# Optimization experiments

Measured on AMD Instinct MI355X. Metric: run time of the kernel, lower is better.

The kernel has to match this reference:

```python
import jax, jax.numpy as jnp
import numpy as np

D_MODEL = 768
D_INNER = 1536   # expand=2
D_STATE = 16
D_CONV = 4
DT_RANK = 48     # ceil(768/16)
B, T, N = 2, 4, 196


def _rmsnorm(x, w, eps=1e-5):
    var = jnp.mean(x * x, axis=-1, keepdims=True)
    return x * jax.lax.rsqrt(var + eps) * w


def _causal_dwconv(x, w, b):
    # x: (b, l, di), w: (di, k) depthwise, causal left-pad k-1
    xc = jnp.swapaxes(x, 1, 2)  # (b, di, l)
    out = jax.lax.conv_general_dilated(
        xc, w[:, None, :], window_strides=(1,), padding=[(D_CONV - 1, 0)],
        feature_group_count=D_INNER, dimension_numbers=('NCH', 'OIH', 'NCH'))
    return jnp.swapaxes(out + b[None, :, None], 1, 2)


def _selective_scan(u, dt, A, Bm, Cm, Dp):
    # u, dt: (b,l,di); Bm, Cm: (b,l,n); A: (di,n); Dp: (di,)
    dA = jnp.exp(dt[..., None] * A)                    # (b,l,di,n)
    dBu = (dt * u)[..., None] * Bm[:, :, None, :]      # (b,l,di,n)

    def step(h, inp):
        dA_t, dBu_t, C_t = inp
        h = dA_t * h + dBu_t                           # (b,di,n)
        return h, jnp.einsum('bdn,bn->bd', h, C_t)

    h0 = jnp.zeros((u.shape[0], D_INNER, D_STATE), u.dtype)
    _, ys = jax.lax.scan(step, h0, (jnp.swapaxes(dA, 0, 1),
                                    jnp.swapaxes(dBu, 0, 1),
                                    jnp.swapaxes(Cm, 0, 1)))
    return jnp.swapaxes(ys, 0, 1) + u * Dp


def _mamba(x, in_w, cw, cb, xp_w, dt_w, dt_b, A_log, Dp, out_w):
    xz = jnp.einsum('blc,ec->ble', x, in_w)            # (b,l,2*di)
    xb, z = jnp.split(xz, 2, axis=-1)
    xb = jax.nn.silu(_causal_dwconv(xb, cw, cb))
    x_dbl = jnp.einsum('bld,ed->ble', xb, xp_w)        # (b,l,dt_rank+2n)
    dt, Bm, Cm = jnp.split(x_dbl, [DT_RANK, DT_RANK + D_STATE], axis=-1)
    dt = jax.nn.softplus(jnp.einsum('blr,dr->bld', dt, dt_w) + dt_b)
    y = _selective_scan(xb, dt, -jnp.exp(A_log), Bm, Cm, Dp)
    y = y * jax.nn.silu(z)
    return jnp.einsum('bld,cd->blc', y, out_w)


def _block(x, i, norm_w, in_proj_w, conv_w, conv_b, x_proj_w, dt_proj_w,
           dt_proj_b, A_log, D, mix_out_w):
    # residual Mamba block: x + mixer(norm(x)); zero-initialized ssm/conv state
    return x + _mamba(_rmsnorm(x, norm_w[i]), in_proj_w[i], conv_w[i], conv_b[i],
                      x_proj_w[i], dt_proj_w[i], dt_proj_b[i], A_log[i], D[i],
                      mix_out_w[i])


def _bimamba(x, norm_w, in_proj_w, conv_w, conv_b, x_proj_w, dt_proj_w,
             dt_proj_b, A_log, D, mix_out_w, gate_w, gate_b, proj_w, proj_b):
    b, t, n, c = x.shape
    xs = x.reshape(b, t * n, c)
    params = (norm_w, in_proj_w, conv_w, conv_b, x_proj_w, dt_proj_w,
              dt_proj_b, A_log, D, mix_out_w)
    out_f = _block(xs, 0, *params)
    flip_t = lambda y: y.reshape(b, t, n, c)[:, ::-1].reshape(b, t * n, c)
    out_b = flip_t(_block(flip_t(xs), 1, *params))
    gate = jax.nn.sigmoid(
        jnp.einsum('blc,dc->bld', jnp.concatenate([out_f, out_b], -1), gate_w)
        + gate_b)
    out = gate * out_f + (1.0 - gate) * out_b
    out = jnp.einsum('bld,cd->blc', out, proj_w) + proj_b
    return out.reshape(b, t, n, c)


def setup_inputs() -> dict:
    key = jax.random.key(0)
    ks = jax.random.split(key, 12)
    s = 0.02
    a_log = jnp.broadcast_to(
        jnp.log(jnp.arange(1, D_STATE + 1, dtype=jnp.float32)),
        (2, D_INNER, D_STATE)).copy()
    return {
        'x': jax.random.normal(ks[0], (B, T, N, D_MODEL), jnp.float32),
        'norm_w': jnp.ones((2, D_MODEL), jnp.float32),
        'in_proj_w': jax.random.normal(ks[1], (2, 2 * D_INNER, D_MODEL), jnp.float32) * s,
        'conv_w': jax.random.normal(ks[2], (2, D_INNER, D_CONV), jnp.float32) * 0.2,
        'conv_b': jnp.zeros((2, D_INNER), jnp.float32),
        'x_proj_w': jax.random.normal(ks[3], (2, DT_RANK + 2 * D_STATE, D_INNER), jnp.float32) * s,
        'dt_proj_w': jax.random.normal(ks[4], (2, D_INNER, DT_RANK), jnp.float32) * s,
        'dt_proj_b': jax.random.normal(ks[5], (2, D_INNER), jnp.float32) * 0.5 - 4.0,
        'A_log': a_log,
        'D': jnp.ones((2, D_INNER), jnp.float32),
        'mix_out_w': jax.random.normal(ks[6], (2, D_MODEL, D_INNER), jnp.float32) * s,
        'gate_w': jax.random.normal(ks[7], (D_MODEL, 2 * D_MODEL), jnp.float32) * s,
        'gate_b': jnp.zeros((D_MODEL,), jnp.float32),
        'proj_w': jax.random.normal(ks[8], (D_MODEL, D_MODEL), jnp.float32) * s,
        'proj_b': jnp.zeros((D_MODEL,), jnp.float32),
    }


def reference(x, norm_w, in_proj_w, conv_w, conv_b, x_proj_w, dt_proj_w,
              dt_proj_b, A_log, D, mix_out_w, gate_w, gate_b, proj_w, proj_b):
    return _bimamba(x, norm_w, in_proj_w, conv_w, conv_b, x_proj_w, dt_proj_w,
                    dt_proj_b, A_log, D, mix_out_w, gate_w, gate_b, proj_w,
                    proj_b)
```

## Files before the change

kernel.cpp:

```cpp
#include <hip/hip_runtime.h>
#include <cstdint>
#include <cstddef>

#define BB 2
#define TT 4
#define NN 196
#define LL (TT*NN)
#define BLr (BB*LL)
#define CM 768
#define DI 1536
#define DS 16
#define DTR 48
#define XD 80
#define GCH 16
#define LC (LL/GCH)
#define NST (2*BB*DI*DS)

typedef short s16x8 __attribute__((ext_vector_type(8)));
typedef float f32x4 __attribute__((ext_vector_type(4)));

static __device__ __forceinline__ float sigmoidf_(float x) {
  return 1.f / (1.f + __expf(-x));
}
static __device__ __forceinline__ unsigned short f2bf(float f) {
  unsigned int u = __float_as_uint(f);
  unsigned int r = (u + 0x7fffu + ((u >> 16) & 1u)) >> 16;
  return (unsigned short)r;
}
static __device__ __forceinline__ float bf2f(unsigned short u) {
  return __uint_as_float(((unsigned int)u) << 16);
}
static __device__ __forceinline__ float softplusf_(float v) {
  return (v > 20.f) ? v : __logf(1.f + __expf(v));
}
static __device__ __forceinline__ void gload_lds16(const void* g, void* l) {
  __builtin_amdgcn_global_load_lds(
      (const __attribute__((address_space(1))) void*)g,
      (__attribute__((address_space(3))) void*)l, 16, 0, 0);
}

#define S_INW  4718592
#define S_OUTW 2359296
#define S_GATW 1179648
#define S_PRJW 589824
#define S_XPW  245760
#define S_DTW  196608
#define E0 S_INW
#define E1 (E0 + S_OUTW)
#define E2 (E1 + S_GATW)
#define E3 (E2 + S_PRJW)
#define E4 (E3 + S_XPW)
#define E5 (E4 + S_DTW)
#define NCAST ((E5)/256)

__global__ __launch_bounds__(256) void pre_k(const float* __restrict__ x,
    const float* __restrict__ nw, unsigned short* __restrict__ xn,
    const float* __restrict__ in_w, const float* __restrict__ out_w,
    const float* __restrict__ gate_w, const float* __restrict__ proj_w,
    const float* __restrict__ xp_w, const float* __restrict__ dt_w,
    unsigned short* __restrict__ dst)
{
  int blk = blockIdx.x;
  if (blk < 2*BLr) {
    int l   = blk % LL;
    int b   = (blk / LL) % BB;
    int dir = blk / (BB*LL);
    int lsrc = l;
    if (dir == 1) { int t = l / NN, n = l % NN; lsrc = (TT-1-t)*NN + n; }
    const float* xp = x + ((size_t)b*LL + lsrc)*CM;
    float s = 0.f;
    for (int c = threadIdx.x; c < CM; c += 256) { float v = xp[c]; s += v*v; }
    #pragma unroll
    for (int off = 32; off > 0; off >>= 1) s += __shfl_down(s, off);
    __shared__ float red[4];
    if ((threadIdx.x & 63) == 0) red[threadIdx.x >> 6] = s;
    __syncthreads();
    float tot = red[0] + red[1] + red[2] + red[3];
    float r = rsqrtf(tot * (1.f/CM) + 1e-5f);
    const float* w = nw + dir*CM;
    unsigned short* o = xn + (size_t)blk*CM;
    for (int c = threadIdx.x; c < CM; c += 256) o[c] = f2bf(xp[c] * r * w[c]);
  } else {
    int i = (blk - 2*BLr)*256 + threadIdx.x;
    float v;
    if (i < E0)       v = in_w[i];
    else if (i < E1)  v = out_w[i - E0];
    else if (i < E2)  v = gate_w[i - E1];
    else if (i < E3)  v = proj_w[i - E2];
    else if (i < E4)  v = xp_w[i - E3];
    else {
      int j = i - E4, r = j >> 6, c = j & 63;
      v = (c < 48) ? dt_w[r*48 + c] : 0.f;
    }
    dst[i] = f2bf(v);
  }
}

template <int BM, int BN>
__device__ __forceinline__ void gemm_core(
    const unsigned short* __restrict__ A, int lda,
    const unsigned short* __restrict__ W, int ldw,
    int M, int N, int K, int m0, int n0,
    short* As, short* Ws, f32x4 (*acc)[BN/32])
{
  const int tid = threadIdx.x;
  const int wv = tid >> 6, lane = tid & 63;
  const int wm0 = (wv >> 1)*(BM/2), wn0 = (wv & 1)*(BN/2);
  const int lm = lane & 15, g = lane >> 4;
  const int r8 = lane >> 3, ch = lane & 7;
  const int chs = ch ^ r8;
  constexpr int MT = BM/32, NT = BN/32;
  for (int k0 = 0; k0 < K; k0 += 64) {
    #pragma unroll
    for (int e = 0; e < BM/32; ++e) {
      int rb = e*32 + wv*8;
      int gr = m0 + rb + r8; if (gr >= M) gr = M - 1;
      gload_lds16(A + (size_t)gr*lda + k0 + chs*8, &As[rb*64 + lane*8]);
    }
    #pragma unroll
    for (int e = 0; e < BN/32; ++e) {
      int rb = e*32 + wv*8;
      int gn = n0 + rb + r8; if (gn >= N) gn = N - 1;
      gload_lds16(W + (size_t)gn*ldw + k0 + chs*8, &Ws[rb*64 + lane*8]);
    }
    __syncthreads();
    #pragma unroll
    for (int s = 0; s < 2; ++s) {
      s16x8 af[MT], bf[NT];
      #pragma unroll
      for (int i = 0; i < MT; ++i) {
        int R = wm0 + i*16 + lm;
        af[i] = *(const s16x8*)(&As[R*64 + (((s*4 + g) ^ (R & 7))*8)]);
      }
      #pragma unroll
      for (int j = 0; j < NT; ++j) {
        int Rn = wn0 + j*16 + lm;
        bf[j] = *(const s16x8*)(&Ws[Rn*64 + (((s*4 + g) ^ (Rn & 7))*8)]);
      }
      #pragma unroll
      for (int i = 0; i < MT; ++i)
        #pragma unroll
        for (int j = 0; j < NT; ++j)
          acc[i][j] = __builtin_amdgcn_mfma_f32_16x16x32_bf16(af[i], bf[j], acc[i][j], 0, 0, 0);
    }
    __syncthreads();
  }
}

__global__ __launch_bounds__(256, 2) void gemm_in_k(
    const unsigned short* __restrict__ xn, const unsigned short* __restrict__ w,
    unsigned short* __restrict__ xzout)
{
  __shared__ short As[128*64];
  __shared__ short Ws[128*64];
  const int dir = blockIdx.z;
  const unsigned short* A = xn + (size_t)dir*BLr*CM;
  const unsigned short* W = w  + (size_t)dir*2*DI*CM;
  unsigned short* C = xzout + (size_t)dir*BLr*2*DI;
  const int m0 = blockIdx.y*128, n0 = blockIdx.x*128;
  f32x4 acc[4][4];
  #pragma unroll
  for (int i = 0; i < 4; ++i)
    #pragma unroll
    for (int j = 0; j < 4; ++j) acc[i][j] = (f32x4){0.f,0.f,0.f,0.f};
  gemm_core<128,128>(A, CM, W, CM, BLr, 2*DI, CM, m0, n0, As, Ws, acc);
  const int tid = threadIdx.x, wv = tid >> 6, lane = tid & 63;
  const int wm0 = (wv >> 1)*64, wn0 = (wv & 1)*64;
  const int lm = lane & 15, g = lane >> 4;
  #pragma unroll
  for (int i = 0; i < 4; ++i) {
    int row = m0 + wm0 + i*16 + g*4;
    #pragma unroll
    for (int j = 0; j < 4; ++j) {
      int col = n0 + wn0 + j*16 + lm;
      #pragma unroll
      for (int r = 0; r < 4; ++r)
        if (row + r < BLr) C[(size_t)(row + r)*2*DI + col] = f2bf(acc[i][j][r]);
    }
  }
}

__global__ __launch_bounds__(256, 4) void gemm_dt_k(
    const unsigned short* __restrict__ xdblb, const unsigned short* __restrict__ w,
    const float* __restrict__ dtb, float* __restrict__ dtv)
{
  __shared__ short As[64*64];
  __shared__ short Ws[128*64];
  const int dir = blockIdx.z;
  const unsigned short* A = xdblb + (size_t)dir*BLr*64;
  const unsigned short* W = w + (size_t)dir*DI*64;
  float* C = dtv + (size_t)dir*BLr*DI;
  const float* bias = dtb + (size_t)dir*DI;
  const int m0 = blockIdx.y*64, n0 = blockIdx.x*128;
  f32x4 acc[2][4];
  #pragma unroll
  for (int i = 0; i < 2; ++i)
    #pragma unroll
    for (int j = 0; j < 4; ++j) acc[i][j] = (f32x4){0.f,0.f,0.f,0.f};
  gemm_core<64,128>(A, 64, W, 64, BLr, DI, 64, m0, n0, As, Ws, acc);
  const int tid = threadIdx.x, wv = tid >> 6, lane = tid & 63;
  const int wm0 = (wv >> 1)*32, wn0 = (wv & 1)*64;
  const int lm = lane & 15, g = lane >> 4;
  #pragma unroll
  for (int i = 0; i < 2; ++i) {
    int row = m0 + wm0 + i*16 + g*4;
    #pragma unroll
    for (int j = 0; j < 4; ++j) {
      int col = n0 + wn0 + j*16 + lm;
      float bv = bias[col];
      #pragma unroll
      for (int r = 0; r < 4; ++r) {
        if (row + r >= BLr) continue;
        C[(size_t)(row + r)*DI + col] = softplusf_(acc[i][j][r] + bv);
      }
    }
  }
}

__global__ __launch_bounds__(256, 4) void gemm_outp_k(
    const unsigned short* __restrict__ yb, const unsigned short* __restrict__ w,
    const float* __restrict__ x, unsigned short* __restrict__ cat)
{
  __shared__ short As[64*64];
  __shared__ short Ws[128*64];
  const int dir = blockIdx.z;
  const unsigned short* A = yb + (size_t)dir*BLr*DI;
  const unsigned short* W = w + (size_t)dir*CM*DI;
  const int m0 = blockIdx.y*64, n0 = blockIdx.x*128;
  f32x4 acc[2][4];
  #pragma unroll
  for (int i = 0; i < 2; ++i)
    #pragma unroll
    for (int j = 0; j < 4; ++j) acc[i][j] = (f32x4){0.f,0.f,0.f,0.f};
  gemm_core<64,128>(A, DI, W, DI, BLr, CM, DI, m0, n0, As, Ws, acc);
  const int tid = threadIdx.x, wv = tid >> 6, lane = tid & 63;
  const int wm0 = (wv >> 1)*32, wn0 = (wv & 1)*64;
  const int lm = lane & 15, g = lane >> 4;
  #pragma unroll
  for (int i = 0; i < 2; ++i) {
    int row = m0 + wm0 + i*16 + g*4;
    #pragma unroll
    for (int j = 0; j < 4; ++j) {
      int col = n0 + wn0 + j*16 + lm;
      #pragma unroll
      for (int r = 0; r < 4; ++r) {
        int rr = row + r;
        if (rr >= BLr) continue;
        int rt = rr;
        if (dir == 1) {
          int l = rr % LL, b = rr / LL;
          int t = l / NN, nn = l % NN;
          rt = b*LL + (TT-1-t)*NN + nn;
        }
        float v = x[(size_t)rt*CM + col] + acc[i][j][r];
        cat[(size_t)rt*(2*CM) + dir*CM + col] = f2bf(v);
      }
    }
  }
}

__global__ __launch_bounds__(256, 4) void gemm_gate_k(
    const unsigned short* __restrict__ cat, const unsigned short* __restrict__ w,
    const float* __restrict__ gb, unsigned short* __restrict__ mixb)
{
  __shared__ short As[64*64];
  __shared__ short Ws[64*64];
  const int m0 = blockIdx.y*64, n0 = blockIdx.x*64;
  f32x4 acc[2][2];
  #pragma unroll
  for (int i = 0; i < 2; ++i)
    #pragma unroll
    for (int j = 0; j < 2; ++j) acc[i][j] = (f32x4){0.f,0.f,0.f,0.f};
  gemm_core<64,64>(cat, 2*CM, w, 2*CM, BLr, CM, 2*CM, m0, n0, As, Ws, acc);
  const int tid = threadIdx.x, wv = tid >> 6, lane = tid & 63;
  const int wm0 = (wv >> 1)*32, wn0 = (wv & 1)*32;
  const int lm = lane & 15, g = lane >> 4;
  #pragma unroll
  for (int i = 0; i < 2; ++i) {
    int row = m0 + wm0 + i*16 + g*4;
    #pragma unroll
    for (int j = 0; j < 2; ++j) {
      int col = n0 + wn0 + j*16 + lm;
      float bv = gb[col];
      #pragma unroll
      for (int r = 0; r < 4; ++r) {
        int rr = row + r;
        if (rr >= BLr) continue;
        float gg = sigmoidf_(acc[i][j][r] + bv);
        float fv = bf2f(cat[(size_t)rr*(2*CM) + col]);
        float bo = bf2f(cat[(size_t)rr*(2*CM) + CM + col]);
        mixb[(size_t)rr*CM + col] = f2bf(gg*fv + (1.f - gg)*bo);
      }
    }
  }
}

__global__ __launch_bounds__(256, 4) void gemm_proj_k(
    const unsigned short* __restrict__ mixb, const unsigned short* __restrict__ w,
    const float* __restrict__ pb, float* __restrict__ out)
{
  __shared__ short As[64*64];
  __shared__ short Ws[64*64];
  const int m0 = blockIdx.y*64, n0 = blockIdx.x*64;
  f32x4 acc[2][2];
  #pragma unroll
  for (int i = 0; i < 2; ++i)
    #pragma unroll
    for (int j = 0; j < 2; ++j) acc[i][j] = (f32x4){0.f,0.f,0.f,0.f};
  gemm_core<64,64>(mixb, CM, w, CM, BLr, CM, CM, m0, n0, As, Ws, acc);
  const int tid = threadIdx.x, wv = tid >> 6, lane = tid & 63;
  const int wm0 = (wv >> 1)*32, wn0 = (wv & 1)*32;
  const int lm = lane & 15, g = lane >> 4;
  #pragma unroll
  for (int i = 0; i < 2; ++i) {
    int row = m0 + wm0 + i*16 + g*4;
    #pragma unroll
    for (int j = 0; j < 2; ++j) {
      int col = n0 + wn0 + j*16 + lm;
      float bv = pb[col];
      #pragma unroll
      for (int r = 0; r < 4; ++r)
        if (row + r < BLr) out[(size_t)(row + r)*CM + col] = acc[i][j][r] + bv;
    }
  }
}

__global__ __launch_bounds__(256, 2) void gemm_xproj(
    const unsigned short* __restrict__ ub, const unsigned short* __restrict__ xpw,
    float* __restrict__ part)
{
  __shared__ short As[128*64];
  __shared__ short Ws[128*64];
  const int ks = blockIdx.x, mt = blockIdx.y, dir = blockIdx.z;
  const unsigned short* A = ub + (size_t)dir*BLr*DI + ks*(DI/8);
  const unsigned short* W = xpw + (size_t)dir*XD*DI + ks*(DI/8);
  const int m0 = mt*128;
  f32x4 acc[4][4];
  #pragma unroll
  for (int i = 0; i < 4; ++i)
    #pragma unroll
    for (int j = 0; j < 4; ++j) acc[i][j] = (f32x4){0.f,0.f,0.f,0.f};
  gemm_core<128,128>(A, DI, W, DI, BLr, XD, DI/8, m0, 0, As, Ws, acc);
  const int tid = threadIdx.x, wv = tid >> 6, lane = tid & 63;
  const int wm0 = (wv >> 1)*64, wn0 = (wv & 1)*64;
  const int lm = lane & 15, g = lane >> 4;
  float* P = part + ((size_t)(dir*8 + ks)*BLr)*XD;
  #pragma unroll
  for (int i = 0; i < 4; ++i) {
    int row = m0 + wm0 + i*16 + g*4;
    #pragma unroll
    for (int j = 0; j < 4; ++j) {
      int col = wn0 + j*16 + lm;
      if (col >= XD) continue;
      #pragma unroll
      for (int r = 0; r < 4; ++r)
        if (row + r < BLr) P[(size_t)(row + r)*XD + col] = acc[i][j][r];
    }
  }
}

__global__ void xreduce_k(const float* __restrict__ part,
    float* __restrict__ xdbl, unsigned short* __restrict__ xdbl_b)
{
  int i = blockIdx.x*256 + threadIdx.x;
  if (i >= 2*BLr*XD) return;
  int c = i % XD;
  int r = i / XD;
  float s = 0.f;
  int dir = r / BLr, row = r % BLr;
  #pragma unroll
  for (int ks = 0; ks < 8; ++ks)
    s += part[((size_t)(dir*8 + ks)*BLr + row)*XD + c];
  xdbl[(size_t)r*XD + c] = s;
  if (c < DTR)      xdbl_b[(size_t)r*64 + c] = f2bf(s);
  else if (c < 64)  xdbl_b[(size_t)r*64 + c] = 0;
}

__global__ __launch_bounds__(256) void conv_silu_k(
    const unsigned short* __restrict__ xz, const float* __restrict__ cw,
    const float* __restrict__ cb, unsigned short* __restrict__ ub)
{
  size_t idx = (size_t)blockIdx.x*256 + threadIdx.x;
  if (idx >= (size_t)2*BLr*DI) return;
  int di  = (int)(idx % DI);
  size_t r = idx / DI;
  int l   = (int)(r % LL);
  int dir = (int)(r / (BB*LL));
  size_t rowbase = r - l;
  const float* w = cw + ((size_t)dir*DI + di)*4;
  float acc = cb[dir*DI + di];
  #pragma unroll
  for (int k = 0; k < 4; ++k) {
    int lp = l - 3 + k;
    if (lp >= 0) acc = fmaf(w[k], bf2f(xz[(rowbase + lp)*(2*DI) + di]), acc);
  }
  float v = acc * sigmoidf_(acc);
  ub[idx] = f2bf(v);
}

__global__ __launch_bounds__(256) void scanA_k(const float* __restrict__ dtv,
    const unsigned short* __restrict__ u, const float* __restrict__ xdbl,
    const float* __restrict__ A_log, float* __restrict__ carry,
    float* __restrict__ Pm)
{
  int bx = blockIdx.x;
  int g = bx & (GCH-1);
  int rest = bx / GCH;
  int dchunk = rest % (DI/64);
  int b   = (rest / (DI/64)) % BB;
  int dir = rest / ((DI/64)*BB);
  int tid = threadIdx.x;
  int dl = tid >> 2, q = tid & 3;
  int d = dchunk*64 + dl;
  size_t rb = ((size_t)dir*BB + b) * LL + (size_t)g*LC;
  const float* dtp = dtv + rb*DI + d;
  const unsigned short* up = u + rb*DI + d;
  const float* xB  = xdbl + rb*XD + DTR + 4*q;
  f32x4 al = *(const f32x4*)(A_log + ((size_t)dir*DI + d)*DS + 4*q);
  float Av[4];
  #pragma unroll
  for (int i = 0; i < 4; ++i) Av[i] = -__expf(al[i]);
  float h[4] = {0.f,0.f,0.f,0.f};
  float S = 0.f;
  float ndt[2], nu[2]; f32x4 nB[2];
  #pragma unroll
  for (int e = 0; e < 2; ++e) {
    ndt[e] = dtp[(size_t)e*DI];
    nu[e]  = bf2f(up[(size_t)e*DI]);
    nB[e]  = *(const f32x4*)(xB + (size_t)e*XD);
  }
  #pragma unroll 2
  for (int j = 0; j < LC; ++j) {
    int s = j & 1;
    float cdt = ndt[s], cu = nu[s];
    f32x4 cB = nB[s];
    int lp = j + 2;
    if (lp < LC) {
      ndt[s] = dtp[(size_t)lp*DI];
      nu[s]  = bf2f(up[(size_t)lp*DI]);
      nB[s]  = *(const f32x4*)(xB + (size_t)lp*XD);
    }
    float du = cdt * cu;
    S += cdt;
    #pragma unroll
    for (int i = 0; i < 4; ++i) {
      float dA = __expf(cdt * Av[i]);
      h[i] = fmaf(dA, h[i], du * cB[i]);
    }
  }
  size_t sid = (((size_t)(dir*BB + b)*DI + d)*DS + 4*q);
  f32x4 hc = {h[0], h[1], h[2], h[3]};
  f32x4 pc = {__expf(Av[0]*S), __expf(Av[1]*S), __expf(Av[2]*S), __expf(Av[3]*S)};
  *(f32x4*)(carry + (size_t)g*NST + sid) = hc;
  *(f32x4*)(Pm    + (size_t)g*NST + sid) = pc;
}

__global__ __launch_bounds__(256) void scanB_k(float* __restrict__ carry,
    const float* __restrict__ Pm)
{
  int sid = blockIdx.x*256 + threadIdx.x;
  float h = 0.f;
  #pragma unroll
  for (int g = 0; g < GCH; ++g) {
    float c = carry[(size_t)g*NST + sid];
    float p = Pm[(size_t)g*NST + sid];
    carry[(size_t)g*NST + sid] = h;
    h = fmaf(p, h, c);
  }
}

__global__ __launch_bounds__(256) void scanC_k(const float* __restrict__ dtv,
    const unsigned short* __restrict__ u, const unsigned short* __restrict__ xz,
    const float* __restrict__ xdbl, const float* __restrict__ A_log,
    const float* __restrict__ Dp, const float* __restrict__ h_in,
    unsigned short* __restrict__ y)
{
  int bx = blockIdx.x;
  int g = bx & (GCH-1);
  int rest = bx / GCH;
  int dchunk = rest % (DI/64);
  int b   = (rest / (DI/64)) % BB;
  int dir = rest / ((DI/64)*BB);
  int tid = threadIdx.x;
  int dl = tid >> 2, q = tid & 3;
  int d = dchunk*64 + dl;
  size_t rb = ((size_t)dir*BB + b) * LL + (size_t)g*LC;
  const float* dtp = dtv + rb*DI + d;
  const unsigned short* up = u + rb*DI + d;
  const unsigned short* zp = xz + rb*(2*DI) + DI + d;
  const float* xB  = xdbl + rb*XD + DTR + 4*q;
  const float* xC  = xB + DS;
  unsigned short* yp = y + rb*DI + d;
  f32x4 al = *(const f32x4*)(A_log + ((size_t)dir*DI + d)*DS + 4*q);
  float Av[4];
  #pragma unroll
  for (int i = 0; i < 4; ++i) Av[i] = -__expf(al[i]);
  float Dd = Dp[dir*DI + d];
  size_t sid = (((size_t)(dir*BB + b)*DI + d)*DS + 4*q);
  f32x4 h4 = *(const f32x4*)(h_in + (size_t)g*NST + sid);
  float h[4] = {h4[0], h4[1], h4[2], h4[3]};
  float ndt[2], nu[2], nz[2]; f32x4 nB[2], nC[2];
  #pragma unroll
  for (int e = 0; e < 2; ++e) {
    ndt[e] = dtp[(size_t)e*DI];
    nu[e]  = bf2f(up[(size_t)e*DI]);
    nz[e]  = bf2f(zp[(size_t)e*(2*DI)]);
    nB[e]  = *(const f32x4*)(xB + (size_t)e*XD);
    nC[e]  = *(const f32x4*)(xC + (size_t)e*XD);
  }
  #pragma unroll 2
  for (int j = 0; j < LC; ++j) {
    int s = j & 1;
    float cdt = ndt[s], cu = nu[s], cz = nz[s];
    f32x4 cB = nB[s], cC = nC[s];
    int lp = j + 2;
    if (lp < LC) {
      ndt[s] = dtp[(size_t)lp*DI];
      nu[s]  = bf2f(up[(size_t)lp*DI]);
      nz[s]  = bf2f(zp[(size_t)lp*(2*DI)]);
      nB[s]  = *(const f32x4*)(xB + (size_t)lp*XD);
      nC[s]  = *(const f32x4*)(xC + (size_t)lp*XD);
    }
    float du = cdt * cu;
    float acc = 0.f;
    #pragma unroll
    for (int i = 0; i < 4; ++i) {
      float dA = __expf(cdt * Av[i]);
      h[i] = fmaf(dA, h[i], du * cB[i]);
      acc = fmaf(h[i], cC[i], acc);
    }
    acc += __shfl_xor(acc, 1);
    acc += __shfl_xor(acc, 2);
    if (q == 0) {
      float yv = (acc + cu * Dd) * (cz * sigmoidf_(cz));
      yp[(size_t)j*DI] = f2bf(yv);
    }
  }
}

extern "C" void kernel_launch(void* const* d_in, const int* in_sizes, int n_in,
                              void* d_out, int out_size, void* d_ws, size_t ws_size,
                              hipStream_t stream)
{
  (void)in_sizes; (void)n_in; (void)out_size; (void)ws_size;
  const float* x      = (const float*)d_in[0];
  const float* norm_w = (const float*)d_in[1];
  const float* in_w   = (const float*)d_in[2];
  const float* conv_w = (const float*)d_in[3];
  const float* conv_b = (const float*)d_in[4];
  const float* xp_w   = (const float*)d_in[5];
  const float* dt_w   = (const float*)d_in[6];
  const float* dt_b   = (const float*)d_in[7];
  const float* A_log  = (const float*)d_in[8];
  const float* Dp     = (const float*)d_in[9];
  const float* out_w  = (const float*)d_in[10];
  const float* gate_w = (const float*)d_in[11];
  const float* gate_b = (const float*)d_in[12];
  const float* proj_w = (const float*)d_in[13];
  const float* proj_b = (const float*)d_in[14];
  float* out = (float*)d_out;
  char* wsb  = (char*)d_ws;

  unsigned short* w_all   = (unsigned short*)(wsb + 0);
  unsigned short* in_w_b  = w_all;
  unsigned short* out_w_b = w_all + E0;
  unsigned short* gate_w_b= w_all + E1;
  unsigned short* proj_w_b= w_all + E2;
  unsigned short* xp_w_b  = w_all + E3;
  unsigned short* dt_w_b  = w_all + E4;
  unsigned short* xz_b = (unsigned short*)(wsb + 18579456);
  unsigned short* ub   = (unsigned short*)(wsb + 37847040);
  float* xdbl  = (float*)(wsb + 57114624);
  float* dtvb  = (float*)(wsb + 58118144);
  unsigned short* y_b = (unsigned short*)(wsb + 77385728);
  unsigned short* tmp = (unsigned short*)(wsb + 87019520);
  unsigned short* cat_b = (unsigned short*)(wsb + 106287104);
  unsigned short* mix_b = (unsigned short*)(wsb + 111104000);

  unsigned short* xn_b   = tmp;
  unsigned short* xdbl_b = tmp;
  float* part  = (float*)(wsb + 0);
  float* carry = (float*)(wsb + 0);
  float* Pmat  = (float*)(wsb + 87019520 + 524288);

  pre_k<<<2*BLr + NCAST, 256, 0, stream>>>(
      x, norm_w, xn_b, in_w, out_w, gate_w, proj_w, xp_w, dt_w, w_all);
  gemm_in_k<<<dim3(3072/128, (BLr+127)/128, 2), 256, 0, stream>>>(
      xn_b, in_w_b, xz_b);
  conv_silu_k<<<(int)(((size_t)2*BLr*DI + 255)/256), 256, 0, stream>>>(
      xz_b, conv_w, conv_b, ub);
  gemm_xproj<<<dim3(8, (BLr+127)/128, 2), 256, 0, stream>>>(ub, xp_w_b, part);
  xreduce_k<<<(2*BLr*XD + 255)/256, 256, 0, stream>>>(part, xdbl, xdbl_b);
  gemm_dt_k<<<dim3(DI/128, (BLr+63)/64, 2), 256, 0, stream>>>(
      xdbl_b, dt_w_b, dt_b, dtvb);
  scanA_k<<<2*BB*(DI/64)*GCH, 256, 0, stream>>>(
      dtvb, ub, xdbl, A_log, carry, Pmat);
  scanB_k<<<NST/256, 256, 0, stream>>>(carry, Pmat);
  scanC_k<<<2*BB*(DI/64)*GCH, 256, 0, stream>>>(
      dtvb, ub, xz_b, xdbl, A_log, Dp, carry, y_b);
  gemm_outp_k<<<dim3(CM/128, (BLr+63)/64, 2), 256, 0, stream>>>(
      y_b, out_w_b, x, cat_b);
  gemm_gate_k<<<dim3(CM/64, (BLr+63)/64, 1), 256, 0, stream>>>(
      cat_b, gate_w_b, gate_b, mix_b);
  gemm_proj_k<<<dim3(CM/64, (BLr+63)/64, 1), 256, 0, stream>>>(
      mix_b, proj_w_b, proj_b, out);
}
```

Baseline: 310.2 us.

## Fuse conv into x_proj GEMM, fold reduction into dt GEMM, single-pass scan

Computes the causal depthwise conv and SiLU while staging the x_proj GEMM A-tile, which removes a separate kernel and a round trip of the activation. The split-K partial sums are reduced inside the dt-projection kernel, which also writes the fp32 x_dbl. The chunked three-kernel scan (local scan, carry propagation, final scan) is replaced by one sequential scan over the full sequence. This drops launches and carry traffic but makes each thread run a serial loop over the whole sequence with far fewer blocks in flight.

Result: slower. 713.9 us (+130.2%).

```diff
diff --git a/kernel.cpp b/kernel.cpp
--- a/kernel.cpp
+++ b/kernel.cpp
@@ -12,9 +12,7 @@
 #define DS 16
 #define DTR 48
 #define XD 80
-#define GCH 16
-#define LC (LL/GCH)
-#define NST (2*BB*DI*DS)
+#define KSL (DI/4)
 
 typedef short s16x8 __attribute__((ext_vector_type(8)));
 typedef float f32x4 __attribute__((ext_vector_type(4)));
@@ -180,27 +178,176 @@
   }
 }
 
-__global__ __launch_bounds__(256, 4) void gemm_dt_k(
-    const unsigned short* __restrict__ xdblb, const unsigned short* __restrict__ w,
-    const float* __restrict__ dtb, float* __restrict__ dtv)
+__global__ __launch_bounds__(256, 2) void convxproj_k(
+    const unsigned short* __restrict__ xz, const float* __restrict__ cw,
+    const float* __restrict__ cb, const unsigned short* __restrict__ xpw,
+    unsigned short* __restrict__ ub, float* __restrict__ part)
+{
+  __shared__ short As[128*64];
+  __shared__ short Ws[128*64];
+  const int ks = blockIdx.x, mt = blockIdx.y, dir = blockIdx.z;
+  const int m0 = mt*128;
+  const int tid = threadIdx.x;
+  const int wv = tid >> 6, lane = tid & 63;
+  const int r8 = lane >> 3, ch = lane & 7;
+  const int chs = ch ^ r8;
+  const int lm = lane & 15, g = lane >> 4;
+  const int wm0 = (wv >> 1)*64, wn0 = (wv & 1)*64;
+  const unsigned short* XZ = xz + (size_t)dir*BLr*(2*DI);
+  const unsigned short* W  = xpw + (size_t)dir*XD*DI + (size_t)ks*KSL;
+  unsigned short* UB = ub + (size_t)dir*BLr*DI;
+  f32x4 acc[4][4];
+  #pragma unroll
+  for (int i = 0; i < 4; ++i)
+    #pragma unroll
+    for (int j = 0; j < 4; ++j) acc[i][j] = (f32x4){0.f,0.f,0.f,0.f};
+
+  for (int k0 = 0; k0 < KSL; k0 += 64) {
+    const int di = ks*KSL + k0 + chs*8;
+    #pragma unroll
+    for (int e = 0; e < 4; ++e) {
+      int rb = e*32 + wv*8;
+      int gn = rb + r8; if (gn >= XD) gn = XD - 1;
+      gload_lds16(W + (size_t)gn*DI + k0 + chs*8, &Ws[rb*64 + lane*8]);
+    }
+    f32x4 w4[8]; float cbv[8];
+    #pragma unroll
+    for (int j = 0; j < 8; ++j) {
+      w4[j]  = *(const f32x4*)(cw + ((size_t)dir*DI + di + j)*4);
+      cbv[j] = cb[dir*DI + di + j];
+    }
+    #pragma unroll
+    for (int e = 0; e < 4; ++e) {
+      int rb = e*32 + wv*8;
+      int gr = m0 + rb + r8; if (gr >= BLr) gr = BLr - 1;
+      int l = gr % LL;
+      s16x8 tap[4];
+      #pragma unroll
+      for (int k = 0; k < 4; ++k) {
+        int lp = l - 3 + k;
+        if (lp >= 0) tap[k] = *(const s16x8*)(XZ + (size_t)(gr - 3 + k)*(2*DI) + di);
+        else         tap[k] = (s16x8){0,0,0,0,0,0,0,0};
+      }
+      s16x8 outv;
+      #pragma unroll
+      for (int j = 0; j < 8; ++j) {
+        float a = cbv[j];
+        #pragma unroll
+        for (int k = 0; k < 4; ++k)
+          a = fmaf(w4[j][k], bf2f((unsigned short)tap[k][j]), a);
+        float v = a * sigmoidf_(a);
+        outv[j] = (short)f2bf(v);
+      }
+      *(s16x8*)(&As[rb*64 + lane*8]) = outv;
+      *(s16x8*)(UB + (size_t)gr*DI + di) = outv;
+    }
+    __syncthreads();
+    #pragma unroll
+    for (int s = 0; s < 2; ++s) {
+      s16x8 af[4], bfr[4];
+      #pragma unroll
+      for (int i = 0; i < 4; ++i) {
+        int R = wm0 + i*16 + lm;
+        af[i] = *(const s16x8*)(&As[R*64 + (((s*4 + g) ^ (R & 7))*8)]);
+      }
+      #pragma unroll
+      for (int j = 0; j < 4; ++j) {
+        int Rn = wn0 + j*16 + lm;
+        bfr[j] = *(const s16x8*)(&Ws[Rn*64 + (((s*4 + g) ^ (Rn & 7))*8)]);
+      }
+      #pragma unroll
+      for (int i = 0; i < 4; ++i)
+        #pragma unroll
+        for (int j = 0; j < 4; ++j)
+          acc[i][j] = __builtin_amdgcn_mfma_f32_16x16x32_bf16(af[i], bfr[j], acc[i][j], 0, 0, 0);
+    }
+    __syncthreads();
+  }
+  float* P = part + ((size_t)(dir*4 + ks)*BLr)*XD;
+  #pragma unroll
+  for (int i = 0; i < 4; ++i) {
+    int row = m0 + wm0 + i*16 + g*4;
+    #pragma unroll
+    for (int j = 0; j < 4; ++j) {
+      int col = wn0 + j*16 + lm;
+      if (col >= XD) continue;
+      #pragma unroll
+      for (int r = 0; r < 4; ++r)
+        if (row + r < BLr) P[(size_t)(row + r)*XD + col] = acc[i][j][r];
+    }
+  }
+}
+
+__global__ __launch_bounds__(256, 4) void dtx_k(
+    const float* __restrict__ part, const unsigned short* __restrict__ dtw,
+    const float* __restrict__ dtb, float* __restrict__ dtv,
+    float* __restrict__ xdbl)
 {
   __shared__ short As[64*64];
   __shared__ short Ws[128*64];
-  const int dir = blockIdx.z;
-  const unsigned short* A = xdblb + (size_t)dir*BLr*64;
-  const unsigned short* W = w + (size_t)dir*DI*64;
+  const int nt = blockIdx.x, mt = blockIdx.y, dir = blockIdx.z;
+  const int m0 = mt*64, n0 = nt*128;
+  const int tid = threadIdx.x;
+  const int wv = tid >> 6, lane = tid & 63;
+  const int r8 = lane >> 3, ch = lane & 7;
+  const int chs = ch ^ r8;
+  const int lm = lane & 15, g = lane >> 4;
+  const int wm0 = (wv >> 1)*32, wn0 = (wv & 1)*64;
+  const float* P0 = part + ((size_t)(dir*4))*BLr*XD;
+  #pragma unroll
+  for (int e = 0; e < 2; ++e) {
+    int rb = e*32 + wv*8;
+    int gr = m0 + rb + r8; if (gr >= BLr) gr = BLr - 1;
+    s16x8 outv;
+    if (chs < 6) {
+      int c = chs*8;
+      f32x4 s0 = {0.f,0.f,0.f,0.f}, s1 = {0.f,0.f,0.f,0.f};
+      #pragma unroll
+      for (int sl = 0; sl < 4; ++sl) {
+        const float* p = P0 + ((size_t)sl*BLr + gr)*XD + c;
+        s0 += *(const f32x4*)(p);
+        s1 += *(const f32x4*)(p + 4);
+      }
+      #pragma unroll
+      for (int j = 0; j < 4; ++j) { outv[j] = (short)f2bf(s0[j]); outv[4+j] = (short)f2bf(s1[j]); }
+    } else {
+      outv = (s16x8){0,0,0,0,0,0,0,0};
+    }
+    *(s16x8*)(&As[rb*64 + lane*8]) = outv;
+  }
+  #pragma unroll
+  for (int e = 0; e < 4; ++e) {
+    int rb = e*32 + wv*8;
+    int gn = n0 + rb + r8;
+    gload_lds16(dtw + (size_t)dir*DI*64 + (size_t)gn*64 + chs*8, &Ws[rb*64 + lane*8]);
+  }
+  __syncthreads();
+  f32x4 acc[2][4];
+  #pragma unroll
+  for (int i = 0; i < 2; ++i)
+    #pragma unroll
+    for (int j = 0; j < 4; ++j) acc[i][j] = (f32x4){0.f,0.f,0.f,0.f};
+  #pragma unroll
+  for (int s = 0; s < 2; ++s) {
+    s16x8 af[2], bfr[4];
+    #pragma unroll
+    for (int i = 0; i < 2; ++i) {
+      int R = wm0 + i*16 + lm;
+      af[i] = *(const s16x8*)(&As[R*64 + (((s*4 + g) ^ (R & 7))*8)]);
+    }
+    #pragma unroll
+    for (int j = 0; j < 4; ++j) {
+      int Rn = wn0 + j*16 + lm;
+      bfr[j] = *(const s16x8*)(&Ws[Rn*64 + (((s*4 + g) ^ (Rn & 7))*8)]);
+    }
+    #pragma unroll
+    for (int i = 0; i < 2; ++i)
+      #pragma unroll
+      for (int j = 0; j < 4; ++j)
+        acc[i][j] = __builtin_amdgcn_mfma_f32_16x16x32_bf16(af[i], bfr[j], acc[i][j], 0, 0, 0);
+  }
   float* C = dtv + (size_t)dir*BLr*DI;
   const float* bias = dtb + (size_t)dir*DI;
-  const int m0 = blockIdx.y*64, n0 = blockIdx.x*128;
-  f32x4 acc[2][4];
-  #pragma unroll
-  for (int i = 0; i < 2; ++i)
-    #pragma unroll
-    for (int j = 0; j < 4; ++j) acc[i][j] = (f32x4){0.f,0.f,0.f,0.f};
-  gemm_core<64,128>(A, 64, W, 64, BLr, DI, 64, m0, n0, As, Ws, acc);
-  const int tid = threadIdx.x, wv = tid >> 6, lane = tid & 63;
-  const int wm0 = (wv >> 1)*32, wn0 = (wv & 1)*64;
-  const int lm = lane & 15, g = lane >> 4;
   #pragma unroll
   for (int i = 0; i < 2; ++i) {
     int row = m0 + wm0 + i*16 + g*4;
@@ -213,6 +360,82 @@
         if (row + r >= BLr) continue;
         C[(size_t)(row + r)*DI + col] = softplusf_(acc[i][j][r] + bv);
       }
+    }
+  }
+  if (nt == 0) {
+    for (int idx = tid; idx < 64*XD; idx += 256) {
+      int row = idx / XD, c = idx % XD;
+      int gr = m0 + row;
+      if (gr >= BLr) continue;
+      float s = 0.f;
+      #pragma unroll
+      for (int sl = 0; sl < 4; ++sl)
+        s += P0[((size_t)sl*BLr + gr)*XD + c];
+      xdbl[((size_t)dir*BLr + gr)*XD + c] = s;
+    }
+  }
+}
+
+__global__ __launch_bounds__(128) void scan_k(const float* __restrict__ dtv,
+    const unsigned short* __restrict__ u, const unsigned short* __restrict__ xz,
+    const float* __restrict__ xdbl, const float* __restrict__ A_log,
+    const float* __restrict__ Dp, unsigned short* __restrict__ y)
+{
+  int bx = blockIdx.x;
+  int dchunk = bx % 48;
+  int b   = (bx / 48) % BB;
+  int dir = bx / (48*BB);
+  int tid = threadIdx.x;
+  int dl = tid >> 2, q = tid & 3;
+  int d = dchunk*32 + dl;
+  size_t rb = ((size_t)dir*BB + b) * LL;
+  const float* dtp = dtv + rb*DI + d;
+  const unsigned short* up = u + rb*DI + d;
+  const unsigned short* zp = xz + rb*(2*DI) + DI + d;
+  const float* xB  = xdbl + rb*XD + DTR + 4*q;
+  const float* xC  = xB + DS;
+  unsigned short* yp = y + rb*DI + d;
+  f32x4 al = *(const f32x4*)(A_log + ((size_t)dir*DI + d)*DS + 4*q);
+  float Av[4];
+  #pragma unroll
+  for (int i = 0; i < 4; ++i) Av[i] = -__expf(al[i]);
+  float Dd = Dp[dir*DI + d];
+  float h[4] = {0.f,0.f,0.f,0.f};
+  float ndt[2], nu[2], nz[2]; f32x4 nB[2], nC[2];
+  #pragma unroll
+  for (int e = 0; e < 2; ++e) {
+    ndt[e] = dtp[(size_t)e*DI];
+    nu[e]  = bf2f(up[(size_t)e*DI]);
+    nz[e]  = bf2f(zp[(size_t)e*(2*DI)]);
+    nB[e]  = *(const f32x4*)(xB + (size_t)e*XD);
+    nC[e]  = *(const f32x4*)(xC + (size_t)e*XD);
+  }
+  #pragma unroll 2
+  for (int j = 0; j < LL; ++j) {
+    int s = j & 1;
+    float cdt = ndt[s], cu = nu[s], cz = nz[s];
+    f32x4 cB = nB[s], cC = nC[s];
+    int lp = j + 2;
+    if (lp < LL) {
+      ndt[s] = dtp[(size_t)lp*DI];
+      nu[s]  = bf2f(up[(size_t)lp*DI]);
+      nz[s]  = bf2f(zp[(size_t)lp*(2*DI)]);
+      nB[s]  = *(const f32x4*)(xB + (size_t)lp*XD);
+      nC[s]  = *(const f32x4*)(xC + (size_t)lp*XD);
+    }
+    float du = cdt * cu;
+    float acc = 0.f;
+    #pragma unroll
+    for (int i = 0; i < 4; ++i) {
+      float dA = __expf(cdt * Av[i]);
+      h[i] = fmaf(dA, h[i], du * cB[i]);
+      acc = fmaf(h[i], cC[i], acc);
+    }
+    acc += __shfl_xor(acc, 1);
+    acc += __shfl_xor(acc, 2);
+    if (q == 0) {
+      float yv = (acc + cu * Dd) * (cz * sigmoidf_(cz));
+      yp[(size_t)j*DI] = f2bf(yv);
     }
   }
 }
@@ -321,219 +544,6 @@
       #pragma unroll
       for (int r = 0; r < 4; ++r)
         if (row + r < BLr) out[(size_t)(row + r)*CM + col] = acc[i][j][r] + bv;
-    }
-  }
-}
-
-__global__ __launch_bounds__(256, 2) void gemm_xproj(
-    const unsigned short* __restrict__ ub, const unsigned short* __restrict__ xpw,
-    float* __restrict__ part)
-{
-  __shared__ short As[128*64];
-  __shared__ short Ws[128*64];
-  const int ks = blockIdx.x, mt = blockIdx.y, dir = blockIdx.z;
-  const unsigned short* A = ub + (size_t)dir*BLr*DI + ks*(DI/8);
-  const unsigned short* W = xpw + (size_t)dir*XD*DI + ks*(DI/8);
-  const int m0 = mt*128;
-  f32x4 acc[4][4];
-  #pragma unroll
-  for (int i = 0; i < 4; ++i)
-    #pragma unroll
-    for (int j = 0; j < 4; ++j) acc[i][j] = (f32x4){0.f,0.f,0.f,0.f};
-  gemm_core<128,128>(A, DI, W, DI, BLr, XD, DI/8, m0, 0, As, Ws, acc);
-  const int tid = threadIdx.x, wv = tid >> 6, lane = tid & 63;
-  const int wm0 = (wv >> 1)*64, wn0 = (wv & 1)*64;
-  const int lm = lane & 15, g = lane >> 4;
-  float* P = part + ((size_t)(dir*8 + ks)*BLr)*XD;
-  #pragma unroll
-  for (int i = 0; i < 4; ++i) {
-    int row = m0 + wm0 + i*16 + g*4;
-    #pragma unroll
-    for (int j = 0; j < 4; ++j) {
-      int col = wn0 + j*16 + lm;
-      if (col >= XD) continue;
-      #pragma unroll
-      for (int r = 0; r < 4; ++r)
-        if (row + r < BLr) P[(size_t)(row + r)*XD + col] = acc[i][j][r];
-    }
-  }
-}
-
-__global__ void xreduce_k(const float* __restrict__ part,
-    float* __restrict__ xdbl, unsigned short* __restrict__ xdbl_b)
-{
-  int i = blockIdx.x*256 + threadIdx.x;
-  if (i >= 2*BLr*XD) return;
-  int c = i % XD;
-  int r = i / XD;
-  float s = 0.f;
-  int dir = r / BLr, row = r % BLr;
-  #pragma unroll
-  for (int ks = 0; ks < 8; ++ks)
-    s += part[((size_t)(dir*8 + ks)*BLr + row)*XD + c];
-  xdbl[(size_t)r*XD + c] = s;
-  if (c < DTR)      xdbl_b[(size_t)r*64 + c] = f2bf(s);
-  else if (c < 64)  xdbl_b[(size_t)r*64 + c] = 0;
-}
-
-__global__ __launch_bounds__(256) void conv_silu_k(
-    const unsigned short* __restrict__ xz, const float* __restrict__ cw,
-    const float* __restrict__ cb, unsigned short* __restrict__ ub)
-{
-  size_t idx = (size_t)blockIdx.x*256 + threadIdx.x;
-  if (idx >= (size_t)2*BLr*DI) return;
-  int di  = (int)(idx % DI);
-  size_t r = idx / DI;
-  int l   = (int)(r % LL);
-  int dir = (int)(r / (BB*LL));
-  size_t rowbase = r - l;
-  const float* w = cw + ((size_t)dir*DI + di)*4;
-  float acc = cb[dir*DI + di];
-  #pragma unroll
-  for (int k = 0; k < 4; ++k) {
-    int lp = l - 3 + k;
-    if (lp >= 0) acc = fmaf(w[k], bf2f(xz[(rowbase + lp)*(2*DI) + di]), acc);
-  }
-  float v = acc * sigmoidf_(acc);
-  ub[idx] = f2bf(v);
-}
-
-__global__ __launch_bounds__(256) void scanA_k(const float* __restrict__ dtv,
-    const unsigned short* __restrict__ u, const float* __restrict__ xdbl,
-    const float* __restrict__ A_log, float* __restrict__ carry,
-    float* __restrict__ Pm)
-{
-  int bx = blockIdx.x;
-  int g = bx & (GCH-1);
-  int rest = bx / GCH;
-  int dchunk = rest % (DI/64);
-  int b   = (rest / (DI/64)) % BB;
-  int dir = rest / ((DI/64)*BB);
-  int tid = threadIdx.x;
-  int dl = tid >> 2, q = tid & 3;
-  int d = dchunk*64 + dl;
-  size_t rb = ((size_t)dir*BB + b) * LL + (size_t)g*LC;
-  const float* dtp = dtv + rb*DI + d;
-  const unsigned short* up = u + rb*DI + d;
-  const float* xB  = xdbl + rb*XD + DTR + 4*q;
-  f32x4 al = *(const f32x4*)(A_log + ((size_t)dir*DI + d)*DS + 4*q);
-  float Av[4];
-  #pragma unroll
-  for (int i = 0; i < 4; ++i) Av[i] = -__expf(al[i]);
-  float h[4] = {0.f,0.f,0.f,0.f};
-  float S = 0.f;
-  float ndt[2], nu[2]; f32x4 nB[2];
-  #pragma unroll
-  for (int e = 0; e < 2; ++e) {
-    ndt[e] = dtp[(size_t)e*DI];
-    nu[e]  = bf2f(up[(size_t)e*DI]);
-    nB[e]  = *(const f32x4*)(xB + (size_t)e*XD);
-  }
-  #pragma unroll 2
-  for (int j = 0; j < LC; ++j) {
-    int s = j & 1;
-    float cdt = ndt[s], cu = nu[s];
-    f32x4 cB = nB[s];
-    int lp = j + 2;
-    if (lp < LC) {
-      ndt[s] = dtp[(size_t)lp*DI];
-      nu[s]  = bf2f(up[(size_t)lp*DI]);
-      nB[s]  = *(const f32x4*)(xB + (size_t)lp*XD);
-    }
-    float du = cdt * cu;
-    S += cdt;
-    #pragma unroll
-    for (int i = 0; i < 4; ++i) {
-      float dA = __expf(cdt * Av[i]);
-      h[i] = fmaf(dA, h[i], du * cB[i]);
-    }
-  }
-  size_t sid = (((size_t)(dir*BB + b)*DI + d)*DS + 4*q);
-  f32x4 hc = {h[0], h[1], h[2], h[3]};
-  f32x4 pc = {__expf(Av[0]*S), __expf(Av[1]*S), __expf(Av[2]*S), __expf(Av[3]*S)};
-  *(f32x4*)(carry + (size_t)g*NST + sid) = hc;
-  *(f32x4*)(Pm    + (size_t)g*NST + sid) = pc;
-}
-
-__global__ __launch_bounds__(256) void scanB_k(float* __restrict__ carry,
-    const float* __restrict__ Pm)
-{
-  int sid = blockIdx.x*256 + threadIdx.x;
-  float h = 0.f;
-  #pragma unroll
-  for (int g = 0; g < GCH; ++g) {
-    float c = carry[(size_t)g*NST + sid];
-    float p = Pm[(size_t)g*NST + sid];
-    carry[(size_t)g*NST + sid] = h;
-    h = fmaf(p, h, c);
-  }
-}
-
-__global__ __launch_bounds__(256) void scanC_k(const float* __restrict__ dtv,
-    const unsigned short* __restrict__ u, const unsigned short* __restrict__ xz,
-    const float* __restrict__ xdbl, const float* __restrict__ A_log,
-    const float* __restrict__ Dp, const float* __restrict__ h_in,
-    unsigned short* __restrict__ y)
-{
-  int bx = blockIdx.x;
-  int g = bx & (GCH-1);
-  int rest = bx / GCH;
-  int dchunk = rest % (DI/64);
-  int b   = (rest / (DI/64)) % BB;
-  int dir = rest / ((DI/64)*BB);
-  int tid = threadIdx.x;
-  int dl = tid >> 2, q = tid & 3;
-  int d = dchunk*64 + dl;
-  size_t rb = ((size_t)dir*BB + b) * LL + (size_t)g*LC;
-  const float* dtp = dtv + rb*DI + d;
-  const unsigned short* up = u + rb*DI + d;
-  const unsigned short* zp = xz + rb*(2*DI) + DI + d;
-  const float* xB  = xdbl + rb*XD + DTR + 4*q;
-  const float* xC  = xB + DS;
-  unsigned short* yp = y + rb*DI + d;
-  f32x4 al = *(const f32x4*)(A_log + ((size_t)dir*DI + d)*DS + 4*q);
-  float Av[4];
-  #pragma unroll
-  for (int i = 0; i < 4; ++i) Av[i] = -__expf(al[i]);
-  float Dd = Dp[dir*DI + d];
-  size_t sid = (((size_t)(dir*BB + b)*DI + d)*DS + 4*q);
-  f32x4 h4 = *(const f32x4*)(h_in + (size_t)g*NST + sid);
-  float h[4] = {h4[0], h4[1], h4[2], h4[3]};
-  float ndt[2], nu[2], nz[2]; f32x4 nB[2], nC[2];
-  #pragma unroll
-  for (int e = 0; e < 2; ++e) {
-    ndt[e] = dtp[(size_t)e*DI];
-    nu[e]  = bf2f(up[(size_t)e*DI]);
-    nz[e]  = bf2f(zp[(size_t)e*(2*DI)]);
-    nB[e]  = *(const f32x4*)(xB + (size_t)e*XD);
-    nC[e]  = *(const f32x4*)(xC + (size_t)e*XD);
-  }
-  #pragma unroll 2
-  for (int j = 0; j < LC; ++j) {
-    int s = j & 1;
-    float cdt = ndt[s], cu = nu[s], cz = nz[s];
-    f32x4 cB = nB[s], cC = nC[s];
-    int lp = j + 2;
-    if (lp < LC) {
-      ndt[s] = dtp[(size_t)lp*DI];
-      nu[s]  = bf2f(up[(size_t)lp*DI]);
-      nz[s]  = bf2f(zp[(size_t)lp*(2*DI)]);
-      nB[s]  = *(const f32x4*)(xB + (size_t)lp*XD);
-      nC[s]  = *(const f32x4*)(xC + (size_t)lp*XD);
-    }
-    float du = cdt * cu;
-    float acc = 0.f;
-    #pragma unroll
-    for (int i = 0; i < 4; ++i) {
-      float dA = __expf(cdt * Av[i]);
-      h[i] = fmaf(dA, h[i], du * cB[i]);
-      acc = fmaf(h[i], cC[i], acc);
-    }
-    acc += __shfl_xor(acc, 1);
-    acc += __shfl_xor(acc, 2);
-    if (q == 0) {
-      float yv = (acc + cu * Dd) * (cz * sigmoidf_(cz));
-      yp[(size_t)j*DI] = f2bf(yv);
     }
   }
 }
@@ -577,27 +587,18 @@
   unsigned short* cat_b = (unsigned short*)(wsb + 106287104);
   unsigned short* mix_b = (unsigned short*)(wsb + 111104000);
 
-  unsigned short* xn_b   = tmp;
-  unsigned short* xdbl_b = tmp;
-  float* part  = (float*)(wsb + 0);
-  float* carry = (float*)(wsb + 0);
-  float* Pmat  = (float*)(wsb + 87019520 + 524288);
+  unsigned short* xn_b = tmp;
+  float* part = (float*)(wsb + 0);
 
   pre_k<<<2*BLr + NCAST, 256, 0, stream>>>(
       x, norm_w, xn_b, in_w, out_w, gate_w, proj_w, xp_w, dt_w, w_all);
   gemm_in_k<<<dim3(3072/128, (BLr+127)/128, 2), 256, 0, stream>>>(
       xn_b, in_w_b, xz_b);
-  conv_silu_k<<<(int)(((size_t)2*BLr*DI + 255)/256), 256, 0, stream>>>(
-      xz_b, conv_w, conv_b, ub);
-  gemm_xproj<<<dim3(8, (BLr+127)/128, 2), 256, 0, stream>>>(ub, xp_w_b, part);
-  xreduce_k<<<(2*BLr*XD + 255)/256, 256, 0, stream>>>(part, xdbl, xdbl_b);
-  gemm_dt_k<<<dim3(DI/128, (BLr+63)/64, 2), 256, 0, stream>>>(
-      xdbl_b, dt_w_b, dt_b, dtvb);
-  scanA_k<<<2*BB*(DI/64)*GCH, 256, 0, stream>>>(
-      dtvb, ub, xdbl, A_log, carry, Pmat);
-  scanB_k<<<NST/256, 256, 0, stream>>>(carry, Pmat);
-  scanC_k<<<2*BB*(DI/64)*GCH, 256, 0, stream>>>(
-      dtvb, ub, xz_b, xdbl, A_log, Dp, carry, y_b);
+  convxproj_k<<<dim3(4, (BLr+127)/128, 2), 256, 0, stream>>>(
+      xz_b, conv_w, conv_b, xp_w_b, ub, part);
+  dtx_k<<<dim3(DI/128, (BLr+63)/64, 2), 256, 0, stream>>>(
+      part, dt_w_b, dt_b, dtvb, xdbl);
+  scan_k<<<2*BB*48, 128, 0, stream>>>(dtvb, ub, xz_b, xdbl, A_log, Dp, y_b);
   gemm_outp_k<<<dim3(CM/128, (BLr+63)/64, 2), 256, 0, stream>>>(
       y_b, out_w_b, x, cat_b);
   gemm_gate_k<<<dim3(CM/64, (BLr+63)/64, 1), 256, 0, stream>>>(
```
